# Optimization experiments

Measured on AMD Instinct MI355X. Metric: run time of the kernel, lower is better.

Reference implementation:

```python
import jax, jax.numpy as jnp
import numpy as np

NUM_HEAD = 8
NUM_BOX = 4
K = 4                      # kernel_size
P = K * K                  # num_point
HEAD_DIM = 32
V_DIM = 256
Q_DIM = 256


def _kernel_indices():
    # even kernel: linspace(-K/2+0.5, K/2-0.5, K), stack (j, i) i.e. (x, y), /K
    idx = np.linspace(-K // 2 + 0.5, K // 2 - 0.5, K)
    i, j = np.meshgrid(idx, idx, indexing='ij')
    return jnp.asarray(np.stack([j, i], axis=-1).reshape(-1, 2) / K, dtype=jnp.float32)


def _bilinear(vm, gx, gy, Hf, Wf):
    # vm: [b,H,Hf*Wf,dh]; gx,gy: [b,H,M] normalized coords in [0,1]
    # grid_sample(2*g-1, align_corners=False, padding_mode='zeros') semantics
    x = gx * Wf - 0.5
    y = gy * Hf - 0.5
    x0 = jnp.floor(x)
    y0 = jnp.floor(y)
    wx1 = x - x0
    wy1 = y - y0

    def corner(xi, yi, w):
        inb = (xi >= 0) & (xi < Wf) & (yi >= 0) & (yi < Hf)
        xi_c = jnp.clip(xi, 0, Wf - 1).astype(jnp.int32)
        yi_c = jnp.clip(yi, 0, Hf - 1).astype(jnp.int32)
        v = jnp.take_along_axis(vm, (yi_c * Wf + xi_c)[..., None], axis=2)
        return v * (w * inb)[..., None]

    return (corner(x0, y0, (1 - wx1) * (1 - wy1))
            + corner(x0 + 1, y0, wx1 * (1 - wy1))
            + corner(x0, y0 + 1, (1 - wx1) * wy1)
            + corner(x0 + 1, y0 + 1, wx1 * wy1))


def _forward(query, value, Hf, Wf, v_mask, v_valid_ratios, ref_windows,
             box_w, box_b, attn_w, attn_b, vproj_w, vproj_b, oproj_w, oproj_b):
    b, l1, _ = query.shape
    l2 = value.shape[1]
    ki = _kernel_indices()  # [P,2]

    value = value @ vproj_w.T + vproj_b
    value = jnp.where(v_mask[..., None], 0.0, value)
    vm = value.reshape(b, l2, NUM_HEAD, HEAD_DIM).transpose(0, 2, 1, 3)  # [b,H,l2,dh]

    off = (query @ box_w.T + box_b).reshape(b, l1, NUM_HEAD, NUM_BOX, 4)
    ref = ref_windows[:, :, None, None, :]                   # [b,l1,1,1,4]
    ref_size = ref[..., jnp.array([2, 3, 2, 3])]
    boxes = ref + off / 8.0 * ref_size                       # [b,l1,H,B,4]
    center = boxes[..., None, :2]
    size = boxes[..., None, 2:]
    grid = center + ki * jax.nn.relu(size)                   # [b,l1,H,B,P,2]
    grid = grid * v_valid_ratios

    # attention weights: [b,l1,H,B,2,2] -> repeat_interleave -> [b,l1,H,B,K,K]
    aw = (query @ attn_w.T + attn_b).reshape(b, l1, NUM_HEAD, NUM_BOX, 2, 2)
    aw = jnp.repeat(jnp.repeat(aw, K // 2, axis=-1), K // 2, axis=-2)
    spatial_w = jax.nn.softmax(aw.reshape(b, l1, NUM_HEAD, NUM_BOX * P), axis=-1)
    level_w = jax.nn.softmax(aw, axis=3).reshape(b, l1, NUM_HEAD, NUM_BOX * P)

    # per-head bilinear sampling at all B*P points per query
    g = grid.transpose(0, 2, 1, 3, 4, 5).reshape(b, NUM_HEAD, -1, 2)  # [b,H,l1*B*P,2]
    sampled = _bilinear(vm, g[..., 0], g[..., 1], Hf, Wf)             # [b,H,M,dh]
    sampled = sampled.reshape(b, NUM_HEAD, l1, NUM_BOX * P, HEAD_DIM)

    out = jnp.einsum('bhlpd,blhp->blhd', sampled, spatial_w).reshape(b, l1, V_DIM)
    output = out @ oproj_w.T + oproj_b
    # mask branch: level softmax (over boxes) weighted aggregate, summed over points
    mout = jnp.einsum('bhlpd,blhp->blhd', sampled, level_w).reshape(b, l1, V_DIM)
    mask_output = mout @ oproj_w.T + oproj_b
    return output, mask_output, aw


def setup_inputs() -> dict:
    key = jax.random.key(0)
    ks = jax.random.split(key, 12)
    b, l1, Hf, Wf = 8, 300, 64, 64
    l2 = Hf * Wf
    d = Q_DIM
    return {
        'query': jax.random.normal(ks[0], (b, l1, d), jnp.float32),
        'value': jax.random.normal(ks[1], (b, l2, V_DIM), jnp.float32),
        'v_shape': np.array([[Hf, Wf]], dtype=np.int64),
        'v_mask': jnp.zeros((b, l2), dtype=bool),
        'v_start_index': np.array([0], dtype=np.int64),
        'v_valid_ratios': jnp.ones((b, 1, 1, 1, 1, 2), jnp.float32),
        'ref_windows': jax.random.uniform(ks[2], (b, l1, 4), jnp.float32, 0.05, 0.6),
        'box_w': 0.02 * jax.random.normal(ks[3], (NUM_BOX * NUM_HEAD * 4, d), jnp.float32),
        'box_b': jax.random.uniform(ks[4], (NUM_HEAD * NUM_BOX * 4,), jnp.float32),
        'attn_w': 0.02 * jax.random.normal(ks[5], (NUM_HEAD * NUM_BOX * 4, d), jnp.float32),
        'attn_b': 0.1 * jax.random.normal(ks[6], (NUM_HEAD * NUM_BOX * 4,), jnp.float32),
        'vproj_w': 0.05 * jax.random.normal(ks[7], (V_DIM, V_DIM), jnp.float32),
        'vproj_b': jnp.zeros((V_DIM,), jnp.float32),
        'oproj_w': 0.05 * jax.random.normal(ks[8], (d, V_DIM), jnp.float32),
        'oproj_b': jnp.zeros((d,), jnp.float32),
    }


def reference(query, value, v_shape, v_mask, v_start_index, v_valid_ratios, ref_windows,
              box_w, box_b, attn_w, attn_b, vproj_w, vproj_b, oproj_w, oproj_b):
    Hf, Wf = int(v_shape[0, 0]), int(v_shape[0, 1])  # single level, static shapes
    return _forward(query, value, Hf, Wf, v_mask, v_valid_ratios, ref_windows,
                    box_w, box_b, attn_w, attn_b, vproj_w, vproj_b, oproj_w, oproj_b)
```

## Files before the change

kernel.cpp:

```cpp
#include <hip/hip_runtime.h>
#include <cstddef>

#define NH   8
#define NB   4
#define HD   32
#define NPIX 4096
#define NBATCH 8
#define NL   300
#define D    256
#define NQ   (NBATCH * NL)

typedef __attribute__((ext_vector_type(4))) float  f32x4;
typedef __attribute__((ext_vector_type(8))) short  bf16x8;

__device__ __forceinline__ unsigned short f2bf(float f) {
    union { float f; unsigned u; } v; v.f = f;
    unsigned r = v.u + 0x7fffu + ((v.u >> 16) & 1u);
    return (unsigned short)(r >> 16);
}
__device__ __forceinline__ float bf2f(unsigned short u) {
    union { unsigned u; float f; } v; v.u = ((unsigned)u) << 16; return v.f;
}
__device__ __forceinline__ unsigned cvtpk(float lo, float hi) {
    unsigned r;
    asm("v_cvt_pk_bf16_f32 %0, %1, %2" : "=v"(r) : "v"(lo), "v"(hi));
    return r;
}
__device__ __forceinline__ bf16x8 pack8c(f32x4 a, f32x4 b) {
    union { unsigned u[4]; bf16x8 v; } r;
    r.u[0] = cvtpk(a[0], a[1]); r.u[1] = cvtpk(a[2], a[3]);
    r.u[2] = cvtpk(b[0], b[1]); r.u[3] = cvtpk(b[2], b[3]);
    return r.v;
}

__global__ __launch_bounds__(512, 4)
void vproj_kernel(const float* __restrict__ value, const float* __restrict__ Wvf,
                  const float* __restrict__ vbias, const unsigned char* __restrict__ mask,
                  unsigned short* __restrict__ vm)
{
    __shared__ __align__(16) short As[64][72];
    __shared__ __align__(16) short Bs[256][72];
    const int tid  = threadIdx.x;
    const int lane = tid & 63, wid = tid >> 6;
    const int wm = wid >> 2, wn = wid & 3;
    const int row0 = blockIdx.x * 64;
    const int l16 = lane & 15, lg = lane >> 4;

    const int sr = tid >> 3, sc8 = (tid & 7) * 8;

    f32x4 acc[2][4] = {};
    f32x4 pA[2], pB[8];

    auto LOADK = [&](int k0) {
        const float* p = value + (size_t)(row0 + sr) * D + k0 + sc8;
        pA[0] = *(const f32x4*)p; pA[1] = *(const f32x4*)(p + 4);
        #pragma unroll
        for (int i = 0; i < 4; ++i) {
            const float* q = Wvf + (size_t)(sr + i * 64) * D + k0 + sc8;
            pB[2 * i] = *(const f32x4*)q; pB[2 * i + 1] = *(const f32x4*)(q + 4);
        }
    };

    LOADK(0);
    #pragma unroll
    for (int ks = 0; ks < 4; ++ks) {
        *(bf16x8*)&As[sr][sc8] = pack8c(pA[0], pA[1]);
        #pragma unroll
        for (int i = 0; i < 4; ++i)
            *(bf16x8*)&Bs[sr + i * 64][sc8] = pack8c(pB[2 * i], pB[2 * i + 1]);
        __syncthreads();
        if (ks < 3) LOADK((ks + 1) * 64);
        #pragma unroll
        for (int kk = 0; kk < 2; ++kk) {
            bf16x8 af[2], bfr[4];
            #pragma unroll
            for (int m = 0; m < 2; ++m)
                af[m] = *(const bf16x8*)&As[wm * 32 + m * 16 + l16][kk * 32 + lg * 8];
            #pragma unroll
            for (int n = 0; n < 4; ++n)
                bfr[n] = *(const bf16x8*)&Bs[wn * 64 + n * 16 + l16][kk * 32 + lg * 8];
            #pragma unroll
            for (int m = 0; m < 2; ++m)
                #pragma unroll
                for (int n = 0; n < 4; ++n)
                    acc[m][n] = __builtin_amdgcn_mfma_f32_16x16x32_bf16(af[m], bfr[n], acc[m][n], 0, 0, 0);
        }
        __syncthreads();
    }
    #pragma unroll
    for (int m = 0; m < 2; ++m) {
        #pragma unroll
        for (int r = 0; r < 4; ++r) {
            const int grow = row0 + wm * 32 + m * 16 + lg * 4 + r;
            const int bb = grow >> 12, pix = grow & (NPIX - 1);
            const float mf = (mask[grow] != 0) ? 0.f : 1.f;
            #pragma unroll
            for (int n = 0; n < 4; ++n) {
                const int gcol = wn * 64 + n * 16 + l16;
                const int h = gcol >> 5, dd = gcol & 31;
                vm[((size_t)(bb * NH + h) * NPIX + pix) * HD + dd] =
                    f2bf(mf * (acc[m][n][r] + vbias[gcol]));
            }
        }
    }
}

__global__ __launch_bounds__(256)
void proj_kernel(const float* __restrict__ query,
                 const float* __restrict__ box_w, const float* __restrict__ box_b,
                 const float* __restrict__ attn_w, const float* __restrict__ attn_b,
                 float* __restrict__ bp, float* __restrict__ ap, float* __restrict__ awo)
{
    __shared__ float As[16][65];
    __shared__ float Bs[16][65];
    const int tid = threadIdx.x;
    const int tr = tid >> 4, tc = tid & 15;
    float acc[4][4] = {};
    const int row0 = blockIdx.x * 64, col0 = blockIdx.y * 64;
    for (int k0 = 0; k0 < D; k0 += 16) {
        #pragma unroll
        for (int i = 0; i < 4; ++i) {
            int idx = tid + i * 256;
            int r = idx >> 4, kk = idx & 15;
            int qrow = min(row0 + r, NQ - 1);
            As[kk][r] = query[(size_t)qrow * D + k0 + kk];
            int c256 = col0 + r;
            const float* src = (c256 < 128) ? (box_w + (size_t)c256 * D)
                                            : (attn_w + (size_t)(c256 - 128) * D);
            Bs[kk][r] = src[k0 + kk];
        }
        __syncthreads();
        #pragma unroll
        for (int kk = 0; kk < 16; ++kk) {
            float a[4], bv[4];
            #pragma unroll
            for (int i = 0; i < 4; ++i) a[i] = As[kk][tr * 4 + i];
            #pragma unroll
            for (int j = 0; j < 4; ++j) bv[j] = Bs[kk][tc * 4 + j];
            #pragma unroll
            for (int i = 0; i < 4; ++i)
                #pragma unroll
                for (int j = 0; j < 4; ++j)
                    acc[i][j] += a[i] * bv[j];
        }
        __syncthreads();
    }
    #pragma unroll
    for (int i = 0; i < 4; ++i) {
        int q = row0 + tr * 4 + i;
        if (q >= NQ) continue;
        #pragma unroll
        for (int j = 0; j < 4; ++j) {
            int col = col0 + tc * 4 + j;
            if (col < 128) {
                bp[(size_t)q * 128 + col] = acc[i][j] + box_b[col];
            } else {
                int rc = col - 128;
                float val = acc[i][j] + attn_b[rc];
                ap[(size_t)q * 128 + rc] = val;
                int h = rc >> 4, bx = (rc >> 2) & 3, rr = (rc >> 1) & 1, cc = rc & 1;
                float* awq = awo + (size_t)q * 512 + (size_t)(h * NB + bx) * 16;
                awq[(2 * rr + 0) * 4 + 2 * cc + 0] = val;
                awq[(2 * rr + 0) * 4 + 2 * cc + 1] = val;
                awq[(2 * rr + 1) * 4 + 2 * cc + 0] = val;
                awq[(2 * rr + 1) * 4 + 2 * cc + 1] = val;
            }
        }
    }
}

__global__ __launch_bounds__(256)
void sample_kernel(const unsigned short* __restrict__ vm, const float* __restrict__ bp,
                   const float* __restrict__ ap, const float* __restrict__ ref_windows,
                   const float* __restrict__ vratio, const int* __restrict__ vshape,
                   const float* __restrict__ oproj_w, const float* __restrict__ oproj_b,
                   float* __restrict__ out1, float* __restrict__ out2)
{
    __shared__ float sbp[128], sap[128], swh[128], lwh[128], sref4[4];
    __shared__ float4 boxdat[32];
    __shared__ int4   O4[512];
    __shared__ float4 W4[512];
    __shared__ float2 SL[512];
    __shared__ __align__(16) float r1s[256], r2s[256];
    const int bid = blockIdx.x, tid = threadIdx.x;
    const int blk = (bid & 7) * NL + (bid >> 3);
    const int bb = blk / NL;
    if (tid < 128) { sbp[tid] = bp[(size_t)blk * 128 + tid]; sap[tid] = ap[(size_t)blk * 128 + tid]; }
    if (tid < 4) sref4[tid] = ref_windows[(size_t)blk * 4 + tid];
    __syncthreads();
    const int Hf = vshape[0], Wf = vshape[1];
    const float Hff = (float)Hf, Wff = (float)Wf;
    const float vr0 = vratio[bb * 2 + 0], vr1 = vratio[bb * 2 + 1];

    if (tid < 128) {
        float a = sap[tid];
        float m = a;
        m = fmaxf(m, __shfl_xor(m, 1));
        m = fmaxf(m, __shfl_xor(m, 2));
        m = fmaxf(m, __shfl_xor(m, 4));
        m = fmaxf(m, __shfl_xor(m, 8));
        float e = expf(a - m);
        float ldv = e + __shfl_xor(e, 4);
        ldv += __shfl_xor(ldv, 8);
        float ss = ldv + __shfl_xor(ldv, 1);
        ss += __shfl_xor(ss, 2);
        swh[tid] = e / (4.f * ss);
        lwh[tid] = e / ldv;
    } else if (tid < 160) {
        int j = tid - 128;
        float o0 = sbp[j * 4 + 0], o1 = sbp[j * 4 + 1];
        float o2 = sbp[j * 4 + 2], o3 = sbp[j * 4 + 3];
        float cx = sref4[0] + o0 * 0.125f * sref4[2];
        float cy = sref4[1] + o1 * 0.125f * sref4[3];
        float rw = fmaxf(sref4[2] + o2 * 0.125f * sref4[2], 0.f);
        float rh = fmaxf(sref4[3] + o3 * 0.125f * sref4[3], 0.f);
        boxdat[j] = make_float4(cx, cy, rw, rh);
    }
    __syncthreads();

    const float kidx[4] = {-0.375f, -0.125f, 0.125f, 0.375f};
    #pragma unroll
    for (int pp = 0; pp < 2; ++pp) {
        const int p = tid + pp * 256;
        const float4 bd = boxdat[p >> 4];
        const int ii = (p >> 2) & 3, jj = p & 3;
        const float gy = (bd.y + kidx[ii] * bd.w) * vr1;
        const float gx = (bd.x + kidx[jj] * bd.z) * vr0;
        const float y = gy * Hff - 0.5f, x = gx * Wff - 0.5f;
        const float y0f = floorf(y), x0f = floorf(x);
        const int iy0 = (int)y0f, ix0 = (int)x0f;
        const float wy1 = y - y0f, wx1 = x - x0f;
        const float wy0 = 1.f - wy1, wx0 = 1.f - wx1;
        const bool y0in = (iy0 >= 0) & (iy0 < Hf);
        const bool y1in = (iy0 + 1 >= 0) & (iy0 + 1 < Hf);
        const bool x0in = (ix0 >= 0) & (ix0 < Wf);
        const bool x1in = (ix0 + 1 >= 0) & (ix0 + 1 < Wf);
        const int yc0 = min(max(iy0, 0), Hf - 1), yc1 = min(max(iy0 + 1, 0), Hf - 1);
        const int xc0 = min(max(ix0, 0), Wf - 1), xc1 = min(max(ix0 + 1, 0), Wf - 1);
        O4[p] = make_int4((yc0 * Wf + xc0) * HD, (yc0 * Wf + xc1) * HD,
                          (yc1 * Wf + xc0) * HD, (yc1 * Wf + xc1) * HD);
        W4[p] = make_float4((y0in & x0in) ? wy0 * wx0 : 0.f,
                            (y0in & x1in) ? wy0 * wx1 : 0.f,
                            (y1in & x0in) ? wy1 * wx0 : 0.f,
                            (y1in & x1in) ? wy1 * wx1 : 0.f);
        const int kpos = ((p >> 2) & 2) | ((p >> 1) & 1);
        const int hk = (p >> 6) * 16 + ((p >> 4) & 3) * 4 + kpos;
        SL[p] = make_float2(swh[hk], lwh[hk]);
    }
    __syncthreads();

    {
        const int h = tid >> 5, dd = tid & 31;
        const unsigned short* base = vm + ((size_t)(bb * NH + h) * NPIX) * HD + dd;
        float acc = 0.f, accm = 0.f;
        #pragma unroll 4
        for (int t = 0; t < 64; ++t) {
            const int p = h * 64 + t;
            const int4 o = O4[p]; const float4 w = W4[p]; const float2 sl = SL[p];
            const float samp = bf2f(base[o.x]) * w.x + bf2f(base[o.y]) * w.y
                             + bf2f(base[o.z]) * w.z + bf2f(base[o.w]) * w.w;
            acc  += samp * sl.x;
            accm += samp * sl.y;
        }
        r1s[tid] = acc;
        r2s[tid] = accm;
    }
    __syncthreads();

    float a1 = oproj_b[tid], a2 = a1;
    const float* wr = oproj_w + (size_t)tid * 256;
    #pragma unroll 8
    for (int v = 0; v < 256; v += 4) {
        const f32x4 wv = *(const f32x4*)(wr + v);
        const f32x4 x1 = *(const f32x4*)&r1s[v];
        const f32x4 x2 = *(const f32x4*)&r2s[v];
        a1 += wv[0] * x1[0] + wv[1] * x1[1] + wv[2] * x1[2] + wv[3] * x1[3];
        a2 += wv[0] * x2[0] + wv[1] * x2[1] + wv[2] * x2[2] + wv[3] * x2[3];
    }
    out1[(size_t)blk * 256 + tid] = a1;
    out2[(size_t)blk * 256 + tid] = a2;
}

extern "C" void kernel_launch(void* const* d_in, const int* in_sizes, int n_in,
                              void* d_out, int out_size, void* d_ws, size_t ws_size,
                              hipStream_t stream)
{
    const float* query        = (const float*)d_in[0];
    const float* value        = (const float*)d_in[1];
    const int*   vshape       = (const int*)d_in[2];
    const unsigned char* vmask= (const unsigned char*)d_in[3];
    const float* vratio       = (const float*)d_in[5];
    const float* refw         = (const float*)d_in[6];
    const float* box_w        = (const float*)d_in[7];
    const float* box_b        = (const float*)d_in[8];
    const float* attn_w       = (const float*)d_in[9];
    const float* attn_b       = (const float*)d_in[10];
    const float* vproj_w      = (const float*)d_in[11];
    const float* vproj_b      = (const float*)d_in[12];
    const float* oproj_w      = (const float*)d_in[13];
    const float* oproj_b      = (const float*)d_in[14];

    unsigned short* vm_b = (unsigned short*)d_ws;
    float* bp = (float*)(vm_b + 8388608);
    float* ap = bp + 307200;

    float* out1 = (float*)d_out;
    float* out2 = out1 + 614400;
    float* awo  = out2 + 614400;

    vproj_kernel<<<512, 512, 0, stream>>>(value, vproj_w, vproj_b, vmask, vm_b);
    proj_kernel<<<dim3(38, 4), 256, 0, stream>>>(query, box_w, box_b, attn_w, attn_b, bp, ap, awo);
    sample_kernel<<<NQ, 256, 0, stream>>>(vm_b, bp, ap, refw, vratio, vshape,
                                          oproj_w, oproj_b, out1, out2);
}
```

Before: 243.0 us.

## Pre-pack output projection weights to transposed bf16 and split vproj tiles

Adds a small kernel that converts oproj_w to bf16 and writes it in a transposed, interleaved layout. In the final projection of sample_kernel, consecutive threads then read contiguous 8-byte chunks instead of each thread striding through its own fp32 row, which gives coalesced and smaller weight reads. Separately, vproj_kernel moves from 512-thread blocks covering all 256 columns to 256-thread blocks covering 128 columns, with twice as many blocks, to cut LDS use per block. The cost is an extra launch, and bf16 weights in the output projection lose some precision.

New measurement: 210.0 us. -13.6%, faster.

```diff
diff --git a/kernel.cpp b/kernel.cpp
--- a/kernel.cpp
+++ b/kernel.cpp
@@ -12,6 +12,7 @@
 
 typedef __attribute__((ext_vector_type(4))) float  f32x4;
 typedef __attribute__((ext_vector_type(8))) short  bf16x8;
+typedef __attribute__((ext_vector_type(4))) unsigned short u16x4;
 
 __device__ __forceinline__ unsigned short f2bf(float f) {
     union { float f; unsigned u; } v; v.f = f;
@@ -33,41 +34,57 @@
     return r.v;
 }
 
-__global__ __launch_bounds__(512, 4)
+__global__ __launch_bounds__(256)
+void wpack_kernel(const float* __restrict__ W, unsigned short* __restrict__ WTP)
+{
+    const int g = blockIdx.x * 256 + threadIdx.x;
+    const int j = g >> 6, v4 = g & 63;
+    const f32x4 w = *(const f32x4*)(W + (size_t)j * 256 + v4 * 4);
+    u16x4 o;
+    o[0] = f2bf(w[0]); o[1] = f2bf(w[1]); o[2] = f2bf(w[2]); o[3] = f2bf(w[3]);
+    *(u16x4*)(WTP + (size_t)v4 * 1024 + j * 4) = o;
+}
+
+__global__ __launch_bounds__(256)
 void vproj_kernel(const float* __restrict__ value, const float* __restrict__ Wvf,
                   const float* __restrict__ vbias, const unsigned char* __restrict__ mask,
                   unsigned short* __restrict__ vm)
 {
     __shared__ __align__(16) short As[64][72];
-    __shared__ __align__(16) short Bs[256][72];
+    __shared__ __align__(16) short Bs[128][72];
     const int tid  = threadIdx.x;
     const int lane = tid & 63, wid = tid >> 6;
-    const int wm = wid >> 2, wn = wid & 3;
-    const int row0 = blockIdx.x * 64;
+    const int wm = wid >> 1, wn = wid & 1;
+    const int mt = blockIdx.x >> 1, nt = blockIdx.x & 1;
+    const int row0 = mt * 64, col0 = nt * 128;
     const int l16 = lane & 15, lg = lane >> 4;
 
-    const int sr = tid >> 3, sc8 = (tid & 7) * 8;
+    const int sr = tid >> 2, sc = (tid & 3) * 16;
+    const int br = tid >> 1, bc = (tid & 1) * 32;
 
     f32x4 acc[2][4] = {};
-    f32x4 pA[2], pB[8];
+    f32x4 pA[4], pB[8];
 
     auto LOADK = [&](int k0) {
-        const float* p = value + (size_t)(row0 + sr) * D + k0 + sc8;
-        pA[0] = *(const f32x4*)p; pA[1] = *(const f32x4*)(p + 4);
+        const float* p = value + (size_t)(row0 + sr) * D + k0 + sc;
+        pA[0] = *(const f32x4*)p;       pA[1] = *(const f32x4*)(p + 4);
+        pA[2] = *(const f32x4*)(p + 8); pA[3] = *(const f32x4*)(p + 12);
+        const float* q = Wvf + (size_t)(col0 + br) * D + k0 + bc;
         #pragma unroll
         for (int i = 0; i < 4; ++i) {
-            const float* q = Wvf + (size_t)(sr + i * 64) * D + k0 + sc8;
-            pB[2 * i] = *(const f32x4*)q; pB[2 * i + 1] = *(const f32x4*)(q + 4);
+            pB[2 * i] = *(const f32x4*)(q + 8 * i);
+            pB[2 * i + 1] = *(const f32x4*)(q + 8 * i + 4);
         }
     };
 
     LOADK(0);
     #pragma unroll
     for (int ks = 0; ks < 4; ++ks) {
-        *(bf16x8*)&As[sr][sc8] = pack8c(pA[0], pA[1]);
+        *(bf16x8*)&As[sr][sc]     = pack8c(pA[0], pA[1]);
+        *(bf16x8*)&As[sr][sc + 8] = pack8c(pA[2], pA[3]);
         #pragma unroll
         for (int i = 0; i < 4; ++i)
-            *(bf16x8*)&Bs[sr + i * 64][sc8] = pack8c(pB[2 * i], pB[2 * i + 1]);
+            *(bf16x8*)&Bs[br][bc + 8 * i] = pack8c(pB[2 * i], pB[2 * i + 1]);
         __syncthreads();
         if (ks < 3) LOADK((ks + 1) * 64);
         #pragma unroll
@@ -96,7 +113,7 @@
             const float mf = (mask[grow] != 0) ? 0.f : 1.f;
             #pragma unroll
             for (int n = 0; n < 4; ++n) {
-                const int gcol = wn * 64 + n * 16 + l16;
+                const int gcol = col0 + wn * 64 + n * 16 + l16;
                 const int h = gcol >> 5, dd = gcol & 31;
                 vm[((size_t)(bb * NH + h) * NPIX + pix) * HD + dd] =
                     f2bf(mf * (acc[m][n][r] + vbias[gcol]));
@@ -173,7 +190,7 @@
 void sample_kernel(const unsigned short* __restrict__ vm, const float* __restrict__ bp,
                    const float* __restrict__ ap, const float* __restrict__ ref_windows,
                    const float* __restrict__ vratio, const int* __restrict__ vshape,
-                   const float* __restrict__ oproj_w, const float* __restrict__ oproj_b,
+                   const unsigned short* __restrict__ WTP, const float* __restrict__ oproj_b,
                    float* __restrict__ out1, float* __restrict__ out2)
 {
     __shared__ float sbp[128], sap[128], swh[128], lwh[128], sref4[4];
@@ -268,14 +285,15 @@
     __syncthreads();
 
     float a1 = oproj_b[tid], a2 = a1;
-    const float* wr = oproj_w + (size_t)tid * 256;
+    const unsigned short* wp = WTP + (size_t)tid * 4;
     #pragma unroll 8
-    for (int v = 0; v < 256; v += 4) {
-        const f32x4 wv = *(const f32x4*)(wr + v);
-        const f32x4 x1 = *(const f32x4*)&r1s[v];
-        const f32x4 x2 = *(const f32x4*)&r2s[v];
-        a1 += wv[0] * x1[0] + wv[1] * x1[1] + wv[2] * x1[2] + wv[3] * x1[3];
-        a2 += wv[0] * x2[0] + wv[1] * x2[1] + wv[2] * x2[2] + wv[3] * x2[3];
+    for (int v4 = 0; v4 < 64; ++v4) {
+        const u16x4 wv = *(const u16x4*)(wp + v4 * 1024);
+        const f32x4 x1 = *(const f32x4*)&r1s[v4 * 4];
+        const f32x4 x2 = *(const f32x4*)&r2s[v4 * 4];
+        const float w0 = bf2f(wv[0]), w1 = bf2f(wv[1]), w2 = bf2f(wv[2]), w3 = bf2f(wv[3]);
+        a1 += w0 * x1[0] + w1 * x1[1] + w2 * x1[2] + w3 * x1[3];
+        a2 += w0 * x2[0] + w1 * x2[1] + w2 * x2[2] + w3 * x2[3];
     }
     out1[(size_t)blk * 256 + tid] = a1;
     out2[(size_t)blk * 256 + tid] = a2;
@@ -301,15 +319,17 @@
     const float* oproj_b      = (const float*)d_in[14];
 
     unsigned short* vm_b = (unsigned short*)d_ws;
-    float* bp = (float*)(vm_b + 8388608);
+    unsigned short* wtp  = vm_b + 8388608;
+    float* bp = (float*)(wtp + 65536);
     float* ap = bp + 307200;
 
     float* out1 = (float*)d_out;
     float* out2 = out1 + 614400;
     float* awo  = out2 + 614400;
 
-    vproj_kernel<<<512, 512, 0, stream>>>(value, vproj_w, vproj_b, vmask, vm_b);
+    wpack_kernel<<<64, 256, 0, stream>>>(oproj_w, wtp);
+    vproj_kernel<<<1024, 256, 0, stream>>>(value, vproj_w, vproj_b, vmask, vm_b);
     proj_kernel<<<dim3(38, 4), 256, 0, stream>>>(query, box_w, box_b, attn_w, attn_b, bp, ap, awo);
     sample_kernel<<<NQ, 256, 0, stream>>>(vm_b, bp, ap, refw, vratio, vshape,
-                                          oproj_w, oproj_b, out1, out2);
-}
+                                          wtp, oproj_b, out1, out2);
+}
```
